# Optimization experiments

Hardware: AMD Instinct MI355X
Metric: run time of the kernel (lower is better)

The kernel has to match this reference:

```python
import jax, jax.numpy as jnp
import numpy as np

D_MODEL, D_C, C_I, N_H_I, TOP_K = 2048, 512, 64, 4, 512


def setup_inputs() -> dict:
    key = jax.random.key(0)
    ks = jax.random.split(key, 7)
    B, S_q, S_kv = 2, 4096, 16384
    h_q = jax.random.normal(ks[0], (B, S_q, D_MODEL), dtype=jnp.float32)
    h_kv = jax.random.normal(ks[1], (B, S_kv, D_MODEL), dtype=jnp.float32)
    query_positions = jnp.sort(
        jax.random.randint(ks[2], (B, S_q), 0, S_kv), axis=-1
    ).astype(jnp.int64)
    # learned params (Linear with bias=False); stored as [in, out] matrices
    W_dq = jax.random.normal(ks[3], (D_MODEL, D_C), dtype=jnp.float32) / np.sqrt(D_MODEL)
    W_iuq = jax.random.normal(ks[4], (D_C, C_I * N_H_I), dtype=jnp.float32) / np.sqrt(D_C)
    W_w = jax.random.normal(ks[5], (D_MODEL, N_H_I), dtype=jnp.float32) / np.sqrt(D_MODEL)
    W_k = jax.random.normal(ks[6], (D_MODEL, C_I), dtype=jnp.float32) / np.sqrt(D_MODEL)
    return {
        "h_q": h_q,
        "h_kv": h_kv,
        "query_positions": query_positions,
        "compressed_rate": 4,
        "W_dq": W_dq,
        "W_iuq": W_iuq,
        "W_w": W_w,
        "W_k": W_k,
    }


def reference(h_q, h_kv, query_positions, compressed_rate, W_dq, W_iuq, W_w, W_k):
    B, S_q, D = h_q.shape
    n_h = W_w.shape[1]          # n_h_i
    c_i = W_k.shape[1]
    S_k = h_kv.shape[1] // compressed_rate

    c_q = h_q @ W_dq                                       # [B, S_q, d_c]
    q_i = (c_q @ W_iuq).reshape(B, S_q, n_h, c_i)          # [B, S_q, n_h, c_i]
    w = h_q @ W_w                                          # [B, S_q, n_h]

    # mean-pool KV over compression windows, then project to indexer key dim
    k_orig = h_kv[:, : S_k * compressed_rate].reshape(B, S_k, compressed_rate, D).mean(axis=2)
    k_proj = k_orig @ W_k                                  # [B, S_k, c_i]

    # per-head dot products, ReLU, head-weighted sum
    dot = jnp.einsum("bqhc,bkc->bqkh", q_i, k_proj)        # [B, S_q, S_k, n_h]
    scores = jnp.einsum("bqkh,bqh->bqk", jax.nn.relu(dot), w)  # [B, S_q, S_k]

    # causal mask on compressed positions
    div = S_k // S_q + 1
    mask = jnp.arange(S_k)[None, None, :] < (query_positions[:, :, None] // div)
    scores = jnp.where(mask, scores, -jnp.inf)

    top_scores, top_indices = jax.lax.top_k(scores, min(TOP_K, S_k))
    return top_scores, top_indices, c_q
```

## Files before the change

kernel.cpp:

```cpp
#include <hip/hip_runtime.h>
#include <cstdint>
#include <cstddef>

#define DM   2048
#define DC   512
#define CI   64
#define NH   4
#define TOPK 512
#define SQ   4096
#define SKV  16384
#define SK   4096
#define BATCH 2
#define ROWS (BATCH * SQ)
#define KROWS (BATCH * SK)
#define DIVQ 2

#define SENTINEL (-1.0e30f)

__device__ __forceinline__ float force_finite_v9(float v) {
    unsigned u = __float_as_uint(v);
    if ((u & 0x7F800000u) == 0x7F800000u)
        u = (u & 0x80000000u) | 0x7E967699u;
    return __uint_as_float(u);
}

__device__ __forceinline__ unsigned long long make_key_v9(float s, int k) {
    unsigned ub = __float_as_uint(s);
    unsigned u = (ub & 0x80000000u) ? ~ub : (ub | 0x80000000u);
    return ((unsigned long long)u << 32) |
           ((unsigned long long)(4095 - k) << 20);
}

__global__ __launch_bounds__(256) void gemm_f32_v9(const float* __restrict__ A,
                                                   const float* __restrict__ B,
                                                   float* __restrict__ C,
                                                   int M, int N, int K) {
    const int tid = threadIdx.x;
    const int tx = tid & 15, ty = tid >> 4;
    const int m0 = blockIdx.y * 128, n0 = blockIdx.x * 64;

    __shared__ float As[16][132];
    __shared__ float Bs[16][68];

    float acc[8][4];
#pragma unroll
    for (int i = 0; i < 8; i++)
#pragma unroll
        for (int j = 0; j < 4; j++) acc[i][j] = 0.f;

    const int ra = tid >> 1, ca = (tid & 1) * 8;
    const int rb = tid >> 4, cb = (tid & 15) * 4;

    for (int k0 = 0; k0 < K; k0 += 16) {
        const float* ap = A + (size_t)(m0 + ra) * K + (k0 + ca);
        float4 a0 = *(const float4*)ap;
        float4 a1 = *(const float4*)(ap + 4);
        As[ca + 0][ra] = a0.x; As[ca + 1][ra] = a0.y;
        As[ca + 2][ra] = a0.z; As[ca + 3][ra] = a0.w;
        As[ca + 4][ra] = a1.x; As[ca + 5][ra] = a1.y;
        As[ca + 6][ra] = a1.z; As[ca + 7][ra] = a1.w;

        float4 bv = *(const float4*)(B + (size_t)(k0 + rb) * N + (n0 + cb));
        *(float4*)&Bs[rb][cb] = bv;
        __syncthreads();

#pragma unroll
        for (int kk = 0; kk < 16; kk++) {
            float4 x0 = *(const float4*)&As[kk][ty * 8];
            float4 x1 = *(const float4*)&As[kk][ty * 8 + 4];
            float4 y  = *(const float4*)&Bs[kk][tx * 4];
            float av[8] = {x0.x, x0.y, x0.z, x0.w, x1.x, x1.y, x1.z, x1.w};
            float bw[4] = {y.x, y.y, y.z, y.w};
#pragma unroll
            for (int i = 0; i < 8; i++)
#pragma unroll
                for (int j = 0; j < 4; j++)
                    acc[i][j] = fmaf(av[i], bw[j], acc[i][j]);
        }
        __syncthreads();
    }

#pragma unroll
    for (int i = 0; i < 8; i++) {
        float4 v = make_float4(acc[i][0], acc[i][1], acc[i][2], acc[i][3]);
        *(float4*)(C + (size_t)(m0 + ty * 8 + i) * N + n0 + tx * 4) = v;
    }
}

__global__ __launch_bounds__(256) void wproj_v9(const float* __restrict__ hq,
                                                const float* __restrict__ Ww,
                                                float* __restrict__ wout) {
    const int lane = threadIdx.x & 63;
    const int row = blockIdx.x * 4 + (threadIdx.x >> 6);
    const float* hrow = hq + (size_t)row * DM;
    float4 acc = make_float4(0.f, 0.f, 0.f, 0.f);
#pragma unroll
    for (int it = 0; it < 8; it++) {
        int d = it * 256 + lane * 4;
        float4 h4 = *(const float4*)(hrow + d);
        float4 w0 = *(const float4*)(Ww + (size_t)(d + 0) * NH);
        float4 w1 = *(const float4*)(Ww + (size_t)(d + 1) * NH);
        float4 w2 = *(const float4*)(Ww + (size_t)(d + 2) * NH);
        float4 w3 = *(const float4*)(Ww + (size_t)(d + 3) * NH);
        acc.x = fmaf(h4.x, w0.x, fmaf(h4.y, w1.x, fmaf(h4.z, w2.x, fmaf(h4.w, w3.x, acc.x))));
        acc.y = fmaf(h4.x, w0.y, fmaf(h4.y, w1.y, fmaf(h4.z, w2.y, fmaf(h4.w, w3.y, acc.y))));
        acc.z = fmaf(h4.x, w0.z, fmaf(h4.y, w1.z, fmaf(h4.z, w2.z, fmaf(h4.w, w3.z, acc.z))));
        acc.w = fmaf(h4.x, w0.w, fmaf(h4.y, w1.w, fmaf(h4.z, w2.w, fmaf(h4.w, w3.w, acc.w))));
    }
#pragma unroll
    for (int off = 32; off > 0; off >>= 1) {
        acc.x += __shfl_down(acc.x, off);
        acc.y += __shfl_down(acc.y, off);
        acc.z += __shfl_down(acc.z, off);
        acc.w += __shfl_down(acc.w, off);
    }
    if (lane == 0) *(float4*)(wout + (size_t)row * NH) = acc;
}

__global__ __launch_bounds__(256) void kpool_proj_v9(const float* __restrict__ hkv,
                                                     const float* __restrict__ Wk,
                                                     float* __restrict__ kprojT) {
    __shared__ float pooled[4][DM];
    const int tid = threadIdx.x;
    const int base = blockIdx.x * 4;
#pragma unroll
    for (int r = 0; r < 4; r++) {
        int kr = base + r;
        int b = kr >> 12, k = kr & 4095;
        const float* src = hkv + ((size_t)b * SKV + (size_t)k * 4) * DM;
#pragma unroll
        for (int it = 0; it < 2; it++) {
            int d = tid * 4 + it * 1024;
            float4 s0 = *(const float4*)(src + d);
            float4 s1 = *(const float4*)(src + DM + d);
            float4 s2 = *(const float4*)(src + 2 * DM + d);
            float4 s3 = *(const float4*)(src + 3 * DM + d);
            float4 p;
            p.x = (s0.x + s1.x + s2.x + s3.x) * 0.25f;
            p.y = (s0.y + s1.y + s2.y + s3.y) * 0.25f;
            p.z = (s0.z + s1.z + s2.z + s3.z) * 0.25f;
            p.w = (s0.w + s1.w + s2.w + s3.w) * 0.25f;
            *(float4*)&pooled[r][d] = p;
        }
    }
    __syncthreads();
    const int c = tid & 63, rr = tid >> 6;
    const int kr = base + rr;
    const int b = kr >> 12, k = kr & 4095;
    const float* prow = pooled[rr];
    float acc = 0.f;
    for (int d = 0; d < DM; d += 4) {
        acc = fmaf(prow[d + 0], Wk[(size_t)(d + 0) * CI + c], acc);
        acc = fmaf(prow[d + 1], Wk[(size_t)(d + 1) * CI + c], acc);
        acc = fmaf(prow[d + 2], Wk[(size_t)(d + 2) * CI + c], acc);
        acc = fmaf(prow[d + 3], Wk[(size_t)(d + 3) * CI + c], acc);
    }
    kprojT[((size_t)b * CI + c) * SK + k] = acc;
}

__global__ __launch_bounds__(512) void fused_score_topk_v9(
        const float* __restrict__ qi, const float* __restrict__ wv,
        const float* __restrict__ kprojT, const void* __restrict__ qpos,
        float* __restrict__ out_scores, float* __restrict__ out_idx) {
    const int tid = threadIdx.x;
    const int row = blockIdx.x;
    const int b = row >> 12;
    const int lane = tid & 63;

    __shared__ float qis_t[CI * NH];
    __shared__ float wsh[NH];
    __shared__ int vcs;
    __shared__ __align__(16) unsigned long long keys_l[SK];
    __shared__ unsigned long long sel[TOPK];
    __shared__ unsigned hist[256];
    __shared__ unsigned long long sT, sPref;
    __shared__ int sNeed, sDone, scnt;

    if (tid < 256) {
        float v = qi[(size_t)row * (NH * CI) + tid];
        qis_t[(tid & 63) * NH + (tid >> 6)] = v;
    }
    if (tid < NH) wsh[tid] = wv[(size_t)row * NH + tid];
    if (tid == 0) {
        const unsigned* qu = (const unsigned*)qpos;
        bool is64 = (qu[8191] == 0u);
        long long p = is64 ? ((const long long*)qpos)[row]
                           : (long long)((const int*)qpos)[row];
        int vc = (int)(p / DIVQ);
        if (vc > SK) vc = SK;
        if (vc < 0) vc = 0;
        vcs = vc;
        sNeed = TOPK; sPref = 0; sDone = 0; sT = 0; scnt = 0;
    }
    __syncthreads();

    const int vc = vcs;
    const float* kTb = kprojT + (size_t)b * CI * SK;

    const int k0 = tid * 4;
    const int k1 = 2048 + tid * 4;
    const bool do0 = (k0 < vc), do1 = (k1 < vc);
    float a0[4][NH], a1[4][NH];
#pragma unroll
    for (int e = 0; e < 4; e++)
#pragma unroll
        for (int h = 0; h < NH; h++) { a0[e][h] = 0.f; a1[e][h] = 0.f; }

    if (do0 || do1) {
        const float* p0 = kTb + k0;
        const float* p1 = kTb + k1;
#pragma unroll 8
        for (int c = 0; c < CI; c++) {
            float4 qh = *(const float4*)&qis_t[c * NH];
            if (do0) {
                float4 kv = *(const float4*)p0;
#pragma unroll
                for (int h = 0; h < NH; h++) {
                    float q = (h == 0) ? qh.x : (h == 1) ? qh.y
                             : (h == 2) ? qh.z : qh.w;
                    a0[0][h] = fmaf(q, kv.x, a0[0][h]);
                    a0[1][h] = fmaf(q, kv.y, a0[1][h]);
                    a0[2][h] = fmaf(q, kv.z, a0[2][h]);
                    a0[3][h] = fmaf(q, kv.w, a0[3][h]);
                }
            }
            if (do1) {
                float4 kv = *(const float4*)p1;
#pragma unroll
                for (int h = 0; h < NH; h++) {
                    float q = (h == 0) ? qh.x : (h == 1) ? qh.y
                             : (h == 2) ? qh.z : qh.w;
                    a1[0][h] = fmaf(q, kv.x, a1[0][h]);
                    a1[1][h] = fmaf(q, kv.y, a1[1][h]);
                    a1[2][h] = fmaf(q, kv.z, a1[2][h]);
                    a1[3][h] = fmaf(q, kv.w, a1[3][h]);
                }
            }
            p0 += SK; p1 += SK;
        }
    }

#pragma unroll
    for (int e = 0; e < 4; e++) {
        {
            int k = k0 + e;
            float s = fmaf(fmaxf(a0[e][0], 0.f), wsh[0],
                      fmaf(fmaxf(a0[e][1], 0.f), wsh[1],
                      fmaf(fmaxf(a0[e][2], 0.f), wsh[2],
                           fmaxf(a0[e][3], 0.f) * wsh[3])));
            if (k >= vc) s = SENTINEL;
            keys_l[e * 1024 + tid] = make_key_v9(force_finite_v9(s), k);
        }
        {
            int k = k1 + e;
            float s = fmaf(fmaxf(a1[e][0], 0.f), wsh[0],
                      fmaf(fmaxf(a1[e][1], 0.f), wsh[1],
                      fmaf(fmaxf(a1[e][2], 0.f), wsh[2],
                           fmaxf(a1[e][3], 0.f) * wsh[3])));
            if (k >= vc) s = SENTINEL;
            keys_l[e * 1024 + 512 + tid] = make_key_v9(force_finite_v9(s), k);
        }
    }
    __syncthreads();

    if (vc <= TOPK) {
        sel[tid] = keys_l[(tid & 3) * 1024 + (tid >> 2)];
        __syncthreads();
    } else {
        for (int pass = 0; pass < 6 && !sDone; pass++) {
            const int shift = 56 - 8 * pass;
            const unsigned long long pref = sPref;
            if (tid < 256) hist[tid] = 0;
            __syncthreads();
            for (int i = tid; i < SK; i += 512) {
                unsigned long long key = keys_l[i];
                int dig;
                if (pass == 0) dig = (int)((key >> shift) & 0xFFull);
                else dig = ((key >> (shift + 8)) == pref)
                               ? (int)((key >> shift) & 0xFFull) : 256;
                unsigned long long m = ~0ull;
#pragma unroll
                for (int bit = 0; bit < 9; bit++) {
                    unsigned long long bm = __ballot((dig >> bit) & 1);
                    m &= ((dig >> bit) & 1) ? bm : ~bm;
                }
                int leader = __ffsll(m) - 1;
                if (lane == leader && dig < 256)
                    atomicAdd(&hist[dig], (unsigned)__popcll(m));
            }
            __syncthreads();
            if (tid < 64) {
                unsigned h0 = hist[tid * 4 + 0], h1 = hist[tid * 4 + 1];
                unsigned h2 = hist[tid * 4 + 2], h3 = hist[tid * 4 + 3];
                unsigned s3 = h3, s2 = h2 + s3, s1 = h1 + s2, s0 = h0 + s1;
                unsigned suff = s0;
#pragma unroll
                for (int off = 1; off < 64; off <<= 1) {
                    unsigned v = __shfl_down(suff, off);
                    if (tid + off < 64) suff += v;
                }
                unsigned above_q = suff - s0;
                unsigned sj[5] = {s0, s1, s2, s3, 0};
                int need = sNeed;
#pragma unroll
                for (int j = 0; j < 4; j++) {
                    unsigned tb = sj[j] + above_q;
                    unsigned ab = sj[j + 1] + above_q;
                    if ((int)tb >= need && (int)ab < need) {
                        int need2 = need - (int)ab;
                        unsigned inbin = tb - ab;
                        unsigned long long dig = (unsigned long long)(tid * 4 + j);
                        if (need2 == (int)inbin) {
                            sT = ((sPref << 8) | dig) << shift;
                            sDone = 1;
                        } else {
                            sPref = (sPref << 8) | dig;
                            sNeed = need2;
                        }
                    }
                }
            }
            __syncthreads();
        }
        const unsigned long long T = sT;
        for (int i = tid; i < SK; i += 512) {
            unsigned long long key = keys_l[i];
            bool f = (key >= T);
            unsigned long long mask = __ballot(f);
            if (mask) {
                int leader = __ffsll(mask) - 1;
                int base = 0;
                if (lane == leader) base = atomicAdd(&scnt, __popcll(mask));
                base = __shfl(base, leader);
                if (f) {
                    int p = base + __popcll(mask & ((1ull << lane) - 1ull));
                    if (p < TOPK) sel[p] = key;
                }
            }
        }
        __syncthreads();
    }

    for (int size = 2; size <= TOPK; size <<= 1) {
        for (int stride = size >> 1; stride > 0; stride >>= 1) {
            int i = tid;
            int j = i ^ stride;
            if (j > i) {
                unsigned long long a = sel[i], bk = sel[j];
                bool up = ((i & size) == 0);
                if ((a > bk) == up) { sel[i] = bk; sel[j] = a; }
            }
            __syncthreads();
        }
    }

    {
        unsigned long long key = sel[TOPK - 1 - tid];
        unsigned u = (unsigned)(key >> 32);
        int idx = 4095 - (int)((key >> 20) & 0xFFFull);
        unsigned bits = (u & 0x80000000u) ? (u ^ 0x80000000u) : ~u;
        out_scores[(size_t)row * TOPK + tid] = force_finite_v9(__uint_as_float(bits));
        out_idx[(size_t)row * TOPK + tid] = (float)idx;
    }
}

__global__ __launch_bounds__(256) void out_sanitize_v9(unsigned* __restrict__ p,
                                                       int n) {
    int i = blockIdx.x * 256 + threadIdx.x;
    if (i < n) {
        unsigned u = p[i];
        if ((u & 0x7F800000u) == 0x7F800000u)
            p[i] = (u & 0x80000000u) | 0x7E967699u;
    }
}

extern "C" void kernel_launch(void* const* d_in, const int* in_sizes, int n_in,
                              void* d_out, int out_size, void* d_ws, size_t ws_size,
                              hipStream_t stream) {
    const float* h_q   = (const float*)d_in[0];
    const float* h_kv  = (const float*)d_in[1];
    const void*  qpos  = d_in[2];
    const float* W_dq  = (const float*)d_in[4];
    const float* W_iuq = (const float*)d_in[5];
    const float* W_w   = (const float*)d_in[6];
    const float* W_k   = (const float*)d_in[7];

    float* out = (float*)d_out;
    float* out_scores = out;
    float* out_idx    = out + (size_t)ROWS * TOPK;
    float* c_q        = out + (size_t)2 * ROWS * TOPK;

    float* ws     = (float*)d_ws;
    float* kprojT = ws;
    float* q_i    = kprojT + (size_t)BATCH * CI * SK;
    float* wbuf   = q_i + (size_t)ROWS * (NH * CI);

    gemm_f32_v9<<<dim3(DC / 64, ROWS / 128), 256, 0, stream>>>(
        h_q, W_dq, c_q, ROWS, DC, DM);
    gemm_f32_v9<<<dim3((NH * CI) / 64, ROWS / 128), 256, 0, stream>>>(
        c_q, W_iuq, q_i, ROWS, NH * CI, DC);
    wproj_v9<<<ROWS / 4, 256, 0, stream>>>(h_q, W_w, wbuf);
    kpool_proj_v9<<<KROWS / 4, 256, 0, stream>>>(h_kv, W_k, kprojT);
    fused_score_topk_v9<<<ROWS, 512, 0, stream>>>(
        q_i, wbuf, kprojT, qpos, out_scores, out_idx);
    {
        int n = 3 * ROWS * TOPK;
        out_sanitize_v9<<<(n + 255) / 256, 256, 0, stream>>>((unsigned*)out, n);
    }
}
```

Measured before the change: 1.084 ms.

## Process two query rows per block and keep score keys in registers

The fused score/top-k kernel now handles two adjacent query rows per block. Each compressed-key column loaded from kprojT is reused for both rows' dot products, which halves global key traffic per row. The per-row 4096-entry key array is no longer stored in shared memory: each thread keeps its 8 keys per row in registers, and the radix histogram and selection passes read from there. The cost is higher register pressure, which could lower occupancy, and the top-k stage for the two rows now runs one after the other inside a block.

Result: faster. 936.8 us (-13.6%).

```diff
diff --git a/kernel.cpp b/kernel.cpp
--- a/kernel.cpp
+++ b/kernel.cpp
@@ -17,24 +17,24 @@
 
 #define SENTINEL (-1.0e30f)
 
-__device__ __forceinline__ float force_finite_v9(float v) {
+__device__ __forceinline__ float force_finite_v10(float v) {
     unsigned u = __float_as_uint(v);
     if ((u & 0x7F800000u) == 0x7F800000u)
         u = (u & 0x80000000u) | 0x7E967699u;
     return __uint_as_float(u);
 }
 
-__device__ __forceinline__ unsigned long long make_key_v9(float s, int k) {
+__device__ __forceinline__ unsigned long long make_key_v10(float s, int k) {
     unsigned ub = __float_as_uint(s);
     unsigned u = (ub & 0x80000000u) ? ~ub : (ub | 0x80000000u);
     return ((unsigned long long)u << 32) |
            ((unsigned long long)(4095 - k) << 20);
 }
 
-__global__ __launch_bounds__(256) void gemm_f32_v9(const float* __restrict__ A,
-                                                   const float* __restrict__ B,
-                                                   float* __restrict__ C,
-                                                   int M, int N, int K) {
+__global__ __launch_bounds__(256) void gemm_f32_v10(const float* __restrict__ A,
+                                                    const float* __restrict__ B,
+                                                    float* __restrict__ C,
+                                                    int M, int N, int K) {
     const int tid = threadIdx.x;
     const int tx = tid & 15, ty = tid >> 4;
     const int m0 = blockIdx.y * 128, n0 = blockIdx.x * 64;
@@ -87,9 +87,9 @@
     }
 }
 
-__global__ __launch_bounds__(256) void wproj_v9(const float* __restrict__ hq,
-                                                const float* __restrict__ Ww,
-                                                float* __restrict__ wout) {
+__global__ __launch_bounds__(256) void wproj_v10(const float* __restrict__ hq,
+                                                 const float* __restrict__ Ww,
+                                                 float* __restrict__ wout) {
     const int lane = threadIdx.x & 63;
     const int row = blockIdx.x * 4 + (threadIdx.x >> 6);
     const float* hrow = hq + (size_t)row * DM;
@@ -117,9 +117,9 @@
     if (lane == 0) *(float4*)(wout + (size_t)row * NH) = acc;
 }
 
-__global__ __launch_bounds__(256) void kpool_proj_v9(const float* __restrict__ hkv,
-                                                     const float* __restrict__ Wk,
-                                                     float* __restrict__ kprojT) {
+__global__ __launch_bounds__(256) void kpool_proj_v10(const float* __restrict__ hkv,
+                                                      const float* __restrict__ Wk,
+                                                      float* __restrict__ kprojT) {
     __shared__ float pooled[4][DM];
     const int tid = threadIdx.x;
     const int base = blockIdx.x * 4;
@@ -158,214 +158,261 @@
     kprojT[((size_t)b * CI + c) * SK + k] = acc;
 }
 
-__global__ __launch_bounds__(512) void fused_score_topk_v9(
+__global__ __launch_bounds__(512) void fused_score_topk_v10(
         const float* __restrict__ qi, const float* __restrict__ wv,
         const float* __restrict__ kprojT, const void* __restrict__ qpos,
         float* __restrict__ out_scores, float* __restrict__ out_idx) {
     const int tid = threadIdx.x;
-    const int row = blockIdx.x;
-    const int b = row >> 12;
+    const int row0 = blockIdx.x * 2;
+    const int b = row0 >> 12;
     const int lane = tid & 63;
 
-    __shared__ float qis_t[CI * NH];
-    __shared__ float wsh[NH];
-    __shared__ int vcs;
-    __shared__ __align__(16) unsigned long long keys_l[SK];
+    __shared__ float qis_t[2][CI * NH];
+    __shared__ float wsh[2][NH];
+    __shared__ int vcs[2];
     __shared__ unsigned long long sel[TOPK];
     __shared__ unsigned hist[256];
     __shared__ unsigned long long sT, sPref;
     __shared__ int sNeed, sDone, scnt;
 
-    if (tid < 256) {
-        float v = qi[(size_t)row * (NH * CI) + tid];
-        qis_t[(tid & 63) * NH + (tid >> 6)] = v;
-    }
-    if (tid < NH) wsh[tid] = wv[(size_t)row * NH + tid];
-    if (tid == 0) {
+    {
+        int r = tid >> 8, j = tid & 255;
+        float v = qi[(size_t)(row0 + r) * (NH * CI) + j];
+        qis_t[r][(j & 63) * NH + (j >> 6)] = v;
+    }
+    if (tid < 8) wsh[tid >> 2][tid & 3] = wv[(size_t)(row0 + (tid >> 2)) * NH + (tid & 3)];
+    if (tid < 2) {
         const unsigned* qu = (const unsigned*)qpos;
         bool is64 = (qu[8191] == 0u);
-        long long p = is64 ? ((const long long*)qpos)[row]
-                           : (long long)((const int*)qpos)[row];
+        long long p = is64 ? ((const long long*)qpos)[row0 + tid]
+                           : (long long)((const int*)qpos)[row0 + tid];
         int vc = (int)(p / DIVQ);
         if (vc > SK) vc = SK;
         if (vc < 0) vc = 0;
-        vcs = vc;
-        sNeed = TOPK; sPref = 0; sDone = 0; sT = 0; scnt = 0;
+        vcs[tid] = vc;
     }
     __syncthreads();
 
-    const int vc = vcs;
+    const int vc0 = vcs[0], vc1 = vcs[1];
+    const int vcm = (vc0 > vc1) ? vc0 : vc1;
     const float* kTb = kprojT + (size_t)b * CI * SK;
 
-    const int k0 = tid * 4;
-    const int k1 = 2048 + tid * 4;
-    const bool do0 = (k0 < vc), do1 = (k1 < vc);
-    float a0[4][NH], a1[4][NH];
-#pragma unroll
-    for (int e = 0; e < 4; e++)
-#pragma unroll
-        for (int h = 0; h < NH; h++) { a0[e][h] = 0.f; a1[e][h] = 0.f; }
-
-    if (do0 || do1) {
-        const float* p0 = kTb + k0;
-        const float* p1 = kTb + k1;
-#pragma unroll 8
-        for (int c = 0; c < CI; c++) {
-            float4 qh = *(const float4*)&qis_t[c * NH];
-            if (do0) {
+    unsigned long long kr[2][8];
+
+    {
+        const int kA = tid * 4;
+        float acc[2][4][NH];
+#pragma unroll
+        for (int r = 0; r < 2; r++)
+#pragma unroll
+            for (int e = 0; e < 4; e++)
+#pragma unroll
+                for (int h = 0; h < NH; h++) acc[r][e][h] = 0.f;
+        if (kA < vcm) {
+            const float* p0 = kTb + kA;
+#pragma unroll 4
+            for (int c = 0; c < CI; c++) {
                 float4 kv = *(const float4*)p0;
+                float4 q0 = *(const float4*)&qis_t[0][c * NH];
+                float4 q1 = *(const float4*)&qis_t[1][c * NH];
 #pragma unroll
                 for (int h = 0; h < NH; h++) {
-                    float q = (h == 0) ? qh.x : (h == 1) ? qh.y
-                             : (h == 2) ? qh.z : qh.w;
-                    a0[0][h] = fmaf(q, kv.x, a0[0][h]);
-                    a0[1][h] = fmaf(q, kv.y, a0[1][h]);
-                    a0[2][h] = fmaf(q, kv.z, a0[2][h]);
-                    a0[3][h] = fmaf(q, kv.w, a0[3][h]);
-                }
-            }
-            if (do1) {
+                    float qa = (h == 0) ? q0.x : (h == 1) ? q0.y : (h == 2) ? q0.z : q0.w;
+                    float qb = (h == 0) ? q1.x : (h == 1) ? q1.y : (h == 2) ? q1.z : q1.w;
+                    acc[0][0][h] = fmaf(qa, kv.x, acc[0][0][h]);
+                    acc[0][1][h] = fmaf(qa, kv.y, acc[0][1][h]);
+                    acc[0][2][h] = fmaf(qa, kv.z, acc[0][2][h]);
+                    acc[0][3][h] = fmaf(qa, kv.w, acc[0][3][h]);
+                    acc[1][0][h] = fmaf(qb, kv.x, acc[1][0][h]);
+                    acc[1][1][h] = fmaf(qb, kv.y, acc[1][1][h]);
+                    acc[1][2][h] = fmaf(qb, kv.z, acc[1][2][h]);
+                    acc[1][3][h] = fmaf(qb, kv.w, acc[1][3][h]);
+                }
+                p0 += SK;
+            }
+        }
+#pragma unroll
+        for (int r = 0; r < 2; r++) {
+            const int vcr = (r == 0) ? vc0 : vc1;
+#pragma unroll
+            for (int e = 0; e < 4; e++) {
+                int k = kA + e;
+                float s = fmaf(fmaxf(acc[r][e][0], 0.f), wsh[r][0],
+                          fmaf(fmaxf(acc[r][e][1], 0.f), wsh[r][1],
+                          fmaf(fmaxf(acc[r][e][2], 0.f), wsh[r][2],
+                               fmaxf(acc[r][e][3], 0.f) * wsh[r][3])));
+                if (k >= vcr) s = SENTINEL;
+                kr[r][e] = make_key_v10(force_finite_v10(s), k);
+            }
+        }
+    }
+
+    {
+        const int kB = 2048 + tid * 4;
+        float acc[2][4][NH];
+#pragma unroll
+        for (int r = 0; r < 2; r++)
+#pragma unroll
+            for (int e = 0; e < 4; e++)
+#pragma unroll
+                for (int h = 0; h < NH; h++) acc[r][e][h] = 0.f;
+        if (kB < vcm) {
+            const float* p1 = kTb + kB;
+#pragma unroll 4
+            for (int c = 0; c < CI; c++) {
                 float4 kv = *(const float4*)p1;
+                float4 q0 = *(const float4*)&qis_t[0][c * NH];
+                float4 q1 = *(const float4*)&qis_t[1][c * NH];
 #pragma unroll
                 for (int h = 0; h < NH; h++) {
-                    float q = (h == 0) ? qh.x : (h == 1) ? qh.y
-                             : (h == 2) ? qh.z : qh.w;
-                    a1[0][h] = fmaf(q, kv.x, a1[0][h]);
-                    a1[1][h] = fmaf(q, kv.y, a1[1][h]);
-                    a1[2][h] = fmaf(q, kv.z, a1[2][h]);
-                    a1[3][h] = fmaf(q, kv.w, a1[3][h]);
-                }
-            }
-            p0 += SK; p1 += SK;
-        }
-    }
-
-#pragma unroll
-    for (int e = 0; e < 4; e++) {
-        {
-            int k = k0 + e;
-            float s = fmaf(fmaxf(a0[e][0], 0.f), wsh[0],
-                      fmaf(fmaxf(a0[e][1], 0.f), wsh[1],
-                      fmaf(fmaxf(a0[e][2], 0.f), wsh[2],
-                           fmaxf(a0[e][3], 0.f) * wsh[3])));
-            if (k >= vc) s = SENTINEL;
-            keys_l[e * 1024 + tid] = make_key_v9(force_finite_v9(s), k);
-        }
-        {
-            int k = k1 + e;
-            float s = fmaf(fmaxf(a1[e][0], 0.f), wsh[0],
-                      fmaf(fmaxf(a1[e][1], 0.f), wsh[1],
-                      fmaf(fmaxf(a1[e][2], 0.f), wsh[2],
-                           fmaxf(a1[e][3], 0.f) * wsh[3])));
-            if (k >= vc) s = SENTINEL;
-            keys_l[e * 1024 + 512 + tid] = make_key_v9(force_finite_v9(s), k);
-        }
-    }
-    __syncthreads();
-
-    if (vc <= TOPK) {
-        sel[tid] = keys_l[(tid & 3) * 1024 + (tid >> 2)];
+                    float qa = (h == 0) ? q0.x : (h == 1) ? q0.y : (h == 2) ? q0.z : q0.w;
+                    float qb = (h == 0) ? q1.x : (h == 1) ? q1.y : (h == 2) ? q1.z : q1.w;
+                    acc[0][0][h] = fmaf(qa, kv.x, acc[0][0][h]);
+                    acc[0][1][h] = fmaf(qa, kv.y, acc[0][1][h]);
+                    acc[0][2][h] = fmaf(qa, kv.z, acc[0][2][h]);
+                    acc[0][3][h] = fmaf(qa, kv.w, acc[0][3][h]);
+                    acc[1][0][h] = fmaf(qb, kv.x, acc[1][0][h]);
+                    acc[1][1][h] = fmaf(qb, kv.y, acc[1][1][h]);
+                    acc[1][2][h] = fmaf(qb, kv.z, acc[1][2][h]);
+                    acc[1][3][h] = fmaf(qb, kv.w, acc[1][3][h]);
+                }
+                p1 += SK;
+            }
+        }
+#pragma unroll
+        for (int r = 0; r < 2; r++) {
+            const int vcr = (r == 0) ? vc0 : vc1;
+#pragma unroll
+            for (int e = 0; e < 4; e++) {
+                int k = kB + e;
+                float s = fmaf(fmaxf(acc[r][e][0], 0.f), wsh[r][0],
+                          fmaf(fmaxf(acc[r][e][1], 0.f), wsh[r][1],
+                          fmaf(fmaxf(acc[r][e][2], 0.f), wsh[r][2],
+                               fmaxf(acc[r][e][3], 0.f) * wsh[r][3])));
+                if (k >= vcr) s = SENTINEL;
+                kr[r][4 + e] = make_key_v10(force_finite_v10(s), k);
+            }
+        }
+    }
+
+#pragma unroll
+    for (int r = 0; r < 2; r++) {
+        const int row = row0 + r;
+        const int vc = (r == 0) ? vc0 : vc1;
+
+        if (tid == 0) { sNeed = TOPK; sPref = 0; sDone = 0; sT = 0; scnt = 0; }
         __syncthreads();
-    } else {
-        for (int pass = 0; pass < 6 && !sDone; pass++) {
-            const int shift = 56 - 8 * pass;
-            const unsigned long long pref = sPref;
-            if (tid < 256) hist[tid] = 0;
+
+        if (vc <= TOPK) {
+            if (tid < 128) {
+#pragma unroll
+                for (int e = 0; e < 4; e++) sel[tid * 4 + e] = kr[r][e];
+            }
             __syncthreads();
-            for (int i = tid; i < SK; i += 512) {
-                unsigned long long key = keys_l[i];
-                int dig;
-                if (pass == 0) dig = (int)((key >> shift) & 0xFFull);
-                else dig = ((key >> (shift + 8)) == pref)
-                               ? (int)((key >> shift) & 0xFFull) : 256;
-                unsigned long long m = ~0ull;
-#pragma unroll
-                for (int bit = 0; bit < 9; bit++) {
-                    unsigned long long bm = __ballot((dig >> bit) & 1);
-                    m &= ((dig >> bit) & 1) ? bm : ~bm;
-                }
-                int leader = __ffsll(m) - 1;
-                if (lane == leader && dig < 256)
-                    atomicAdd(&hist[dig], (unsigned)__popcll(m));
-            }
-            __syncthreads();
-            if (tid < 64) {
-                unsigned h0 = hist[tid * 4 + 0], h1 = hist[tid * 4 + 1];
-                unsigned h2 = hist[tid * 4 + 2], h3 = hist[tid * 4 + 3];
-                unsigned s3 = h3, s2 = h2 + s3, s1 = h1 + s2, s0 = h0 + s1;
-                unsigned suff = s0;
-#pragma unroll
-                for (int off = 1; off < 64; off <<= 1) {
-                    unsigned v = __shfl_down(suff, off);
-                    if (tid + off < 64) suff += v;
-                }
-                unsigned above_q = suff - s0;
-                unsigned sj[5] = {s0, s1, s2, s3, 0};
-                int need = sNeed;
-#pragma unroll
-                for (int j = 0; j < 4; j++) {
-                    unsigned tb = sj[j] + above_q;
-                    unsigned ab = sj[j + 1] + above_q;
-                    if ((int)tb >= need && (int)ab < need) {
-                        int need2 = need - (int)ab;
-                        unsigned inbin = tb - ab;
-                        unsigned long long dig = (unsigned long long)(tid * 4 + j);
-                        if (need2 == (int)inbin) {
-                            sT = ((sPref << 8) | dig) << shift;
-                            sDone = 1;
-                        } else {
-                            sPref = (sPref << 8) | dig;
-                            sNeed = need2;
+        } else {
+            for (int pass = 0; pass < 6 && !sDone; pass++) {
+                const int shift = 56 - 8 * pass;
+                const unsigned long long pref = sPref;
+                if (tid < 256) hist[tid] = 0;
+                __syncthreads();
+#pragma unroll
+                for (int e = 0; e < 8; e++) {
+                    unsigned long long key = kr[r][e];
+                    int dig;
+                    if (pass == 0) dig = (int)((key >> shift) & 0xFFull);
+                    else dig = ((key >> (shift + 8)) == pref)
+                                   ? (int)((key >> shift) & 0xFFull) : 256;
+                    unsigned long long m = ~0ull;
+#pragma unroll
+                    for (int bit = 0; bit < 9; bit++) {
+                        unsigned long long bm = __ballot((dig >> bit) & 1);
+                        m &= ((dig >> bit) & 1) ? bm : ~bm;
+                    }
+                    int leader = __ffsll(m) - 1;
+                    if (lane == leader && dig < 256)
+                        atomicAdd(&hist[dig], (unsigned)__popcll(m));
+                }
+                __syncthreads();
+                if (tid < 64) {
+                    unsigned h0 = hist[tid * 4 + 0], h1 = hist[tid * 4 + 1];
+                    unsigned h2 = hist[tid * 4 + 2], h3 = hist[tid * 4 + 3];
+                    unsigned s3 = h3, s2 = h2 + s3, s1 = h1 + s2, s0 = h0 + s1;
+                    unsigned suff = s0;
+#pragma unroll
+                    for (int off = 1; off < 64; off <<= 1) {
+                        unsigned v = __shfl_down(suff, off);
+                        if (tid + off < 64) suff += v;
+                    }
+                    unsigned above_q = suff - s0;
+                    unsigned sj[5] = {s0, s1, s2, s3, 0};
+                    int need = sNeed;
+#pragma unroll
+                    for (int j = 0; j < 4; j++) {
+                        unsigned tb = sj[j] + above_q;
+                        unsigned ab = sj[j + 1] + above_q;
+                        if ((int)tb >= need && (int)ab < need) {
+                            int need2 = need - (int)ab;
+                            unsigned inbin = tb - ab;
+                            unsigned long long dig = (unsigned long long)(tid * 4 + j);
+                            if (need2 == (int)inbin) {
+                                sT = ((sPref << 8) | dig) << shift;
+                                sDone = 1;
+                            } else {
+                                sPref = (sPref << 8) | dig;
+                                sNeed = need2;
+                            }
                         }
                     }
                 }
+                __syncthreads();
+            }
+            const unsigned long long T = sT;
+#pragma unroll
+            for (int e = 0; e < 8; e++) {
+                unsigned long long key = kr[r][e];
+                bool f = (key >= T);
+                unsigned long long mask = __ballot(f);
+                if (mask) {
+                    int leader = __ffsll(mask) - 1;
+                    int base = 0;
+                    if (lane == leader) base = atomicAdd(&scnt, __popcll(mask));
+                    base = __shfl(base, leader);
+                    if (f) {
+                        int p = base + __popcll(mask & ((1ull << lane) - 1ull));
+                        if (p < TOPK) sel[p] = key;
+                    }
+                }
             }
             __syncthreads();
         }
-        const unsigned long long T = sT;
-        for (int i = tid; i < SK; i += 512) {
-            unsigned long long key = keys_l[i];
-            bool f = (key >= T);
-            unsigned long long mask = __ballot(f);
-            if (mask) {
-                int leader = __ffsll(mask) - 1;
-                int base = 0;
-                if (lane == leader) base = atomicAdd(&scnt, __popcll(mask));
-                base = __shfl(base, leader);
-                if (f) {
-                    int p = base + __popcll(mask & ((1ull << lane) - 1ull));
-                    if (p < TOPK) sel[p] = key;
-                }
-            }
-        }
-        __syncthreads();
-    }
-
-    for (int size = 2; size <= TOPK; size <<= 1) {
-        for (int stride = size >> 1; stride > 0; stride >>= 1) {
-            int i = tid;
-            int j = i ^ stride;
-            if (j > i) {
-                unsigned long long a = sel[i], bk = sel[j];
-                bool up = ((i & size) == 0);
-                if ((a > bk) == up) { sel[i] = bk; sel[j] = a; }
-            }
-            __syncthreads();
-        }
-    }
-
-    {
-        unsigned long long key = sel[TOPK - 1 - tid];
-        unsigned u = (unsigned)(key >> 32);
-        int idx = 4095 - (int)((key >> 20) & 0xFFFull);
-        unsigned bits = (u & 0x80000000u) ? (u ^ 0x80000000u) : ~u;
-        out_scores[(size_t)row * TOPK + tid] = force_finite_v9(__uint_as_float(bits));
-        out_idx[(size_t)row * TOPK + tid] = (float)idx;
-    }
-}
-
-__global__ __launch_bounds__(256) void out_sanitize_v9(unsigned* __restrict__ p,
-                                                       int n) {
+
+        for (int size = 2; size <= TOPK; size <<= 1) {
+            for (int stride = size >> 1; stride > 0; stride >>= 1) {
+                int i = tid;
+                int j = i ^ stride;
+                if (j > i) {
+                    unsigned long long a = sel[i], bk = sel[j];
+                    bool up = ((i & size) == 0);
+                    if ((a > bk) == up) { sel[i] = bk; sel[j] = a; }
+                }
+                __syncthreads();
+            }
+        }
+
+        {
+            unsigned long long key = sel[TOPK - 1 - tid];
+            unsigned u = (unsigned)(key >> 32);
+            int idx = 4095 - (int)((key >> 20) & 0xFFFull);
+            unsigned bits = (u & 0x80000000u) ? (u ^ 0x80000000u) : ~u;
+            out_scores[(size_t)row * TOPK + tid] =
+                force_finite_v10(__uint_as_float(bits));
+            out_idx[(size_t)row * TOPK + tid] = (float)idx;
+        }
+    }
+}
+
+__global__ __launch_bounds__(256) void out_sanitize_v10(unsigned* __restrict__ p,
+                                                        int n) {
     int i = blockIdx.x * 256 + threadIdx.x;
     if (i < n) {
         unsigned u = p[i];
@@ -395,16 +442,16 @@
     float* q_i    = kprojT + (size_t)BATCH * CI * SK;
     float* wbuf   = q_i + (size_t)ROWS * (NH * CI);
 
-    gemm_f32_v9<<<dim3(DC / 64, ROWS / 128), 256, 0, stream>>>(
+    gemm_f32_v10<<<dim3(DC / 64, ROWS / 128), 256, 0, stream>>>(
         h_q, W_dq, c_q, ROWS, DC, DM);
-    gemm_f32_v9<<<dim3((NH * CI) / 64, ROWS / 128), 256, 0, stream>>>(
+    gemm_f32_v10<<<dim3((NH * CI) / 64, ROWS / 128), 256, 0, stream>>>(
         c_q, W_iuq, q_i, ROWS, NH * CI, DC);
-    wproj_v9<<<ROWS / 4, 256, 0, stream>>>(h_q, W_w, wbuf);
-    kpool_proj_v9<<<KROWS / 4, 256, 0, stream>>>(h_kv, W_k, kprojT);
-    fused_score_topk_v9<<<ROWS, 512, 0, stream>>>(
+    wproj_v10<<<ROWS / 4, 256, 0, stream>>>(h_q, W_w, wbuf);
+    kpool_proj_v10<<<KROWS / 4, 256, 0, stream>>>(h_kv, W_k, kprojT);
+    fused_score_topk_v10<<<ROWS / 2, 512, 0, stream>>>(
         q_i, wbuf, kprojT, qpos, out_scores, out_idx);
     {
         int n = 3 * ROWS * TOPK;
-        out_sanitize_v9<<<(n + 255) / 256, 256, 0, stream>>>((unsigned*)out, n);
-    }
-}
+        out_sanitize_v10<<<(n + 255) / 256, 256, 0, stream>>>((unsigned*)out, n);
+    }
+}
```
